# Kernel optimization log

Hardware: AMD Instinct MI355X
Metric: run time of the kernel (lower is better)

Reference implementation:

```python
import jax, jax.numpy as jnp
import numpy as np

NUM_HEADS = 16
HEAD_DIM = 128
NUM_KV_HEADS = 8
NUM_KV_GROUPS = 2
HIDDEN = 2048
SCALE = 0.5  # hardcoded in the original SDPA call


def _fixed_sincos_pos(E, H):
    # matches ReusedProjReconstructor._fixed_sincos_pos (H even here)
    half = H // 2
    freq = jnp.exp(-jnp.log(jnp.float32(10000.0)) * jnp.arange(half, dtype=jnp.float32) / half)
    pos = jnp.arange(E, dtype=jnp.float32)[:, None]
    ang = pos * freq[None, :]
    return jnp.concatenate([jnp.sin(ang), jnp.cos(ang)], axis=1)  # [E, H]


def setup_inputs() -> dict:
    key = jax.random.key(0)
    ks = jax.random.split(key, 8)
    B, M, H = 4, 2048, HIDDEN
    kv_dim = NUM_KV_HEADS * HEAD_DIM
    s = 0.02
    return {
        "mem_act": jax.random.normal(ks[0], (B, M, H), jnp.float32),
        "Wq": jax.random.normal(ks[1], (H, H), jnp.float32) * s,
        "bq": jax.random.normal(ks[2], (H,), jnp.float32) * s,
        "Wk": jax.random.normal(ks[3], (kv_dim, H), jnp.float32) * s,
        "bk": jax.random.normal(ks[4], (kv_dim,), jnp.float32) * s,
        "Wv": jax.random.normal(ks[5], (kv_dim, H), jnp.float32) * s,
        "bv": jax.random.normal(ks[6], (kv_dim,), jnp.float32) * s,
        "Wo": jax.random.normal(ks[7], (H, H), jnp.float32) * s,
        "E": 2048,
    }


def reference(mem_act, Wq, bq, Wk, bk, Wv, bv, Wo, E):
    B, M, H = mem_act.shape
    # positional query hidden, shared across batch (q_ln is Identity)
    q_hidden = _fixed_sincos_pos(E, H).astype(mem_act.dtype)  # [E, H]
    q = (q_hidden @ Wq.T + bq).reshape(E, NUM_HEADS, HEAD_DIM)          # [E, nh, hd]
    k = (mem_act @ Wk.T + bk).reshape(B, M, NUM_KV_HEADS, HEAD_DIM)     # [B, M, nkv, hd]
    v = (mem_act @ Wv.T + bv).reshape(B, M, NUM_KV_HEADS, HEAD_DIM)
    # GQA: repeat kv heads (repeat_interleave over head dim)
    k = jnp.repeat(k, NUM_KV_GROUPS, axis=2)  # [B, M, nh, hd]
    v = jnp.repeat(v, NUM_KV_GROUPS, axis=2)
    # non-causal SDPA with scale=0.5, query broadcast over batch
    scores = jnp.einsum("ehd,bmhd->bhem", q, k) * SCALE  # [B, nh, E, M]
    attn = jax.nn.softmax(scores, axis=-1)
    out = jnp.einsum("bhem,bmhd->behd", attn, v).reshape(B, E, H)
    pred = out @ Wo.T  # o_proj (no bias, Qwen2 style)
    return pred
```

## Files before the change

### kernel.cpp

```cpp
#include <hip/hip_runtime.h>
#include <hip/hip_bf16.h>

typedef __attribute__((ext_vector_type(8))) short short8;
typedef __attribute__((ext_vector_type(4))) float f32x4;
typedef __attribute__((ext_vector_type(16))) float f32x16;
typedef unsigned short ushort_t;

__device__ __forceinline__ unsigned short f2bf(float x) {
    unsigned int u = __builtin_bit_cast(unsigned int, x);
    unsigned int r = (u + 0x7fffu + ((u >> 16) & 1u)) >> 16;
    return (unsigned short)r;
}

__device__ __forceinline__ void gload_lds16(const ushort_t* g, ushort_t* l) {
    __builtin_amdgcn_global_load_lds(
        (const __attribute__((address_space(1))) void*)g,
        (__attribute__((address_space(3))) void*)l, 16, 0, 0);
}

#define MFMA16(A, B, C) __builtin_amdgcn_mfma_f32_16x16x32_bf16((A), (B), (C), 0, 0, 0)
#define MFMA32(A, B, C) __builtin_amdgcn_mfma_f32_32x32x16_bf16((A), (B), (C), 0, 0, 0)

__global__ __launch_bounds__(256) void prep_all(const float* __restrict__ im,
                                                const float* __restrict__ iq,
                                                const float* __restrict__ ik,
                                                const float* __restrict__ iv,
                                                const float* __restrict__ io,
                                                ushort_t* __restrict__ om,
                                                ushort_t* __restrict__ oq,
                                                ushort_t* __restrict__ ok,
                                                ushort_t* __restrict__ ov,
                                                ushort_t* __restrict__ oo,
                                                ushort_t* __restrict__ qh) {
    const int bid = blockIdx.x;
    if (bid < 14336) {
        long i = ((long)bid * 256 + threadIdx.x) << 3;
        const float* s;
        ushort_t* d;
        if (i < 16777216)      { s = im + i;              d = om + i; }
        else if (i < 20971520) { s = iq + (i - 16777216); d = oq + (i - 16777216); }
        else if (i < 23068672) { s = ik + (i - 20971520); d = ok + (i - 20971520); }
        else if (i < 25165824) { s = iv + (i - 23068672); d = ov + (i - 23068672); }
        else                   { s = io + (i - 25165824); d = oo + (i - 25165824); }
        const float4* p = (const float4*)s;
        float4 a = p[0], b = p[1];
        short8 o;
        o[0] = (short)f2bf(a.x); o[1] = (short)f2bf(a.y);
        o[2] = (short)f2bf(a.z); o[3] = (short)f2bf(a.w);
        o[4] = (short)f2bf(b.x); o[5] = (short)f2bf(b.y);
        o[6] = (short)f2bf(b.z); o[7] = (short)f2bf(b.w);
        *(short8*)d = o;
    } else {
        int idx = (bid - 14336) * 256 + threadIdx.x;
        int e = idx >> 10, i = idx & 1023;
        float freq = __expf(-9.2103403719761836f * (float)i * (1.0f / 1024.0f));
        float ang = (float)e * freq;
        float rev = ang * 0.15915494309189535f;
        rev -= floorf(rev);
        float sv, cv;
        asm("v_sin_f32 %0, %1" : "=v"(sv) : "v"(rev));
        asm("v_cos_f32 %0, %1" : "=v"(cv) : "v"(rev));
        qh[(size_t)e * 2048 + i]        = f2bf(sv);
        qh[(size_t)e * 2048 + 1024 + i] = f2bf(cv);
    }
}

__global__ __launch_bounds__(256, 2) void gemm_q(const ushort_t* __restrict__ A,
                                                 const ushort_t* __restrict__ Bw,
                                                 const float* __restrict__ bias,
                                                 ushort_t* __restrict__ Cout,
                                                 int M, int N, int K) {
    __shared__ ushort_t As[4][128 * 32];
    __shared__ ushort_t Bs[4][128 * 32];
    const int tid = threadIdx.x, lane = tid & 63;
    const int wid = tid >> 6;
    const int q5 = lane & 31, hi = lane >> 5;
    const int wm = wid >> 1, wn = wid & 1;
    const int nbn = N >> 7;
    const int nwg = gridDim.x;
    const int swz = (blockIdx.x & 7) * (nwg >> 3) + (blockIdx.x >> 3);
    const int bm = swz / nbn, bn = swz % nbn;
    const int row0 = bm << 7, col0 = bn << 7;
    const int NT = K >> 5;

    f32x16 acc[2][2];
#pragma unroll
    for (int mi = 0; mi < 2; ++mi)
#pragma unroll
        for (int nj = 0; nj < 2; ++nj)
#pragma unroll
            for (int rr = 0; rr < 16; ++rr) acc[mi][nj][rr] = 0.f;

    auto STAGE_HALF = [&](int buf, int kt, int i) {
        const int k0 = kt << 5;
        const int fb = (i * 256 + tid) << 4;
        const int rp = fb >> 7;
        const int bo = ((fb >> 4) & 7) ^ (rp & 7);
        const int row = rp * 2 + (bo >> 2);
        const int kc = (bo & 3) << 3;
        gload_lds16(A  + (size_t)(row0 + row) * K + k0 + kc, &As[buf][0] + (fb >> 1));
        gload_lds16(Bw + (size_t)(col0 + row) * K + k0 + kc, &Bs[buf][0] + (fb >> 1));
    };

    STAGE_HALF(0, 0, 0); STAGE_HALF(0, 0, 1);
    STAGE_HALF(1, 1, 0); STAGE_HALF(1, 1, 1);
    STAGE_HALF(2, 2, 0); STAGE_HALF(2, 2, 1);
    asm volatile("s_waitcnt vmcnt(8)" ::: "memory");
    __builtin_amdgcn_sched_barrier(0);
    __builtin_amdgcn_s_barrier();
    __builtin_amdgcn_sched_barrier(0);

    for (int t = 0; t < NT; ++t) {
        const int buf = t & 3;
        const char* Ab = (const char*)&As[buf][0];
        const char* Bb = (const char*)&Bs[buf][0];
#pragma unroll
        for (int ph = 0; ph < 2; ++ph) {
            short8 af[2], bfr[2];
#pragma unroll
            for (int nj = 0; nj < 2; ++nj) {
                const int col = wn * 64 + nj * 32 + q5;
                const int rp = col >> 1;
                const int blk = (((col & 1) << 2) + ph * 2 + hi) ^ (rp & 7);
                bfr[nj] = *(const short8*)(Bb + rp * 128 + blk * 16);
            }
#pragma unroll
            for (int mi = 0; mi < 2; ++mi) {
                const int row = wm * 64 + mi * 32 + q5;
                const int rp = row >> 1;
                const int blk = (((row & 1) << 2) + ph * 2 + hi) ^ (rp & 7);
                af[mi] = *(const short8*)(Ab + rp * 128 + blk * 16);
            }
            if (t + 3 < NT) STAGE_HALF((t + 3) & 3, t + 3, ph);
            __builtin_amdgcn_s_setprio(1);
#pragma unroll
            for (int mi = 0; mi < 2; ++mi)
#pragma unroll
                for (int nj = 0; nj < 2; ++nj)
                    acc[mi][nj] = MFMA32(af[mi], bfr[nj], acc[mi][nj]);
            __builtin_amdgcn_s_setprio(0);
        }

        if (t + 3 < NT) {
            asm volatile("s_waitcnt vmcnt(8)" ::: "memory");
        } else if (t + 2 < NT) {
            asm volatile("s_waitcnt vmcnt(4)" ::: "memory");
        } else if (t + 1 < NT) {
            asm volatile("s_waitcnt vmcnt(0)" ::: "memory");
        }
        if (t + 1 < NT) {
            __builtin_amdgcn_sched_barrier(0);
            __builtin_amdgcn_s_barrier();
            __builtin_amdgcn_sched_barrier(0);
        }
    }

#pragma unroll
    for (int mi = 0; mi < 2; ++mi)
#pragma unroll
        for (int nj = 0; nj < 2; ++nj) {
            const int col = col0 + wn * 64 + nj * 32 + q5;
            const float bv = bias[col];
#pragma unroll
            for (int rr = 0; rr < 16; ++rr) {
                const int row = row0 + wm * 64 + mi * 32 + (rr & 3) + 8 * (rr >> 2) + 4 * hi;
                Cout[(size_t)row * N + col] = f2bf((acc[mi][nj][rr] + bv) * 0.5f);
            }
        }
}

template <int EPI>
__global__ __launch_bounds__(512, 1) void gemm256(const ushort_t* __restrict__ A,
                                                  const ushort_t* __restrict__ Bw,
                                                  const float* __restrict__ b0,
                                                  const float* __restrict__ b1,
                                                  void* __restrict__ C0,
                                                  void* __restrict__ C1,
                                                  int M, int N, int K) {
    __shared__ ushort_t As[4][256 * 32];
    __shared__ ushort_t Bs[4][256 * 32];
    const int tid = threadIdx.x, lane = tid & 63;
    const int wid = tid >> 6;
    const int q5 = lane & 31, hi = lane >> 5;
    const int wm = wid >> 2, wn = wid & 3;
    const int nbn = N >> 8;
    const int nwg = gridDim.x;
    const int swz = (blockIdx.x & 7) * (nwg >> 3) + (blockIdx.x >> 3);
    const int bm = swz / nbn, bn = swz % nbn;
    const int row0 = bm << 8, col0 = bn << 8;
    const int NT = K >> 5;

    f32x16 acc[4][2];
#pragma unroll
    for (int mi = 0; mi < 4; ++mi)
#pragma unroll
        for (int nj = 0; nj < 2; ++nj)
#pragma unroll
            for (int rr = 0; rr < 16; ++rr) acc[mi][nj][rr] = 0.f;

    auto STAGE_HALF = [&](int buf, int kt, int i) {
        const int k0 = kt << 5;
        const int fb = (i * 512 + tid) << 4;
        const int rp = fb >> 7;
        const int bo = ((fb >> 4) & 7) ^ (rp & 7);
        const int row = rp * 2 + (bo >> 2);
        const int kc = (bo & 3) << 3;
        gload_lds16(A  + (size_t)(row0 + row) * K + k0 + kc, &As[buf][0] + (fb >> 1));
        gload_lds16(Bw + (size_t)(col0 + row) * K + k0 + kc, &Bs[buf][0] + (fb >> 1));
    };

    STAGE_HALF(0, 0, 0); STAGE_HALF(0, 0, 1);
    STAGE_HALF(1, 1, 0); STAGE_HALF(1, 1, 1);
    STAGE_HALF(2, 2, 0); STAGE_HALF(2, 2, 1);
    asm volatile("s_waitcnt vmcnt(8)" ::: "memory");
    __builtin_amdgcn_sched_barrier(0);
    __builtin_amdgcn_s_barrier();
    __builtin_amdgcn_sched_barrier(0);

    for (int t = 0; t < NT; ++t) {
        const int buf = t & 3;
        const char* Ab = (const char*)&As[buf][0];
        const char* Bb = (const char*)&Bs[buf][0];
#pragma unroll
        for (int ph = 0; ph < 2; ++ph) {
            short8 af[4], bfr[2];
#pragma unroll
            for (int nj = 0; nj < 2; ++nj) {
                const int col = wn * 64 + nj * 32 + q5;
                const int rp = col >> 1;
                const int blk = (((col & 1) << 2) + ph * 2 + hi) ^ (rp & 7);
                bfr[nj] = *(const short8*)(Bb + rp * 128 + blk * 16);
            }
#pragma unroll
            for (int mi = 0; mi < 4; ++mi) {
                const int row = wm * 128 + mi * 32 + q5;
                const int rp = row >> 1;
                const int blk = (((row & 1) << 2) + ph * 2 + hi) ^ (rp & 7);
                af[mi] = *(const short8*)(Ab + rp * 128 + blk * 16);
            }
            if (t + 3 < NT) STAGE_HALF((t + 3) & 3, t + 3, ph);
            __builtin_amdgcn_s_setprio(1);
#pragma unroll
            for (int mi = 0; mi < 4; ++mi)
#pragma unroll
                for (int nj = 0; nj < 2; ++nj)
                    acc[mi][nj] = MFMA32(af[mi], bfr[nj], acc[mi][nj]);
            __builtin_amdgcn_s_setprio(0);
        }

        if (t + 3 < NT) {
            asm volatile("s_waitcnt vmcnt(8)" ::: "memory");
        } else if (t + 2 < NT) {
            asm volatile("s_waitcnt vmcnt(4)" ::: "memory");
        } else if (t + 1 < NT) {
            asm volatile("s_waitcnt vmcnt(0)" ::: "memory");
        }
        if (t + 1 < NT) {
            __builtin_amdgcn_sched_barrier(0);
            __builtin_amdgcn_s_barrier();
            __builtin_amdgcn_sched_barrier(0);
        }
    }

#pragma unroll
    for (int mi = 0; mi < 4; ++mi)
#pragma unroll
        for (int nj = 0; nj < 2; ++nj) {
            const int col = col0 + wn * 64 + nj * 32 + q5;
            if (EPI == 2) {
                float* outp = (float*)C0;
#pragma unroll
                for (int rr = 0; rr < 16; ++rr) {
                    const int row = row0 + wm * 128 + mi * 32 + (rr & 3) + 8 * (rr >> 2) + 4 * hi;
                    outp[(size_t)row * N + col] = acc[mi][nj][rr];
                }
            } else {
                if (col < 1024) {
                    const float bv = b0[col];
                    ushort_t* Kp = (ushort_t*)C0;
#pragma unroll
                    for (int rr = 0; rr < 16; ++rr) {
                        const int row = row0 + wm * 128 + mi * 32 + (rr & 3) + 8 * (rr >> 2) + 4 * hi;
                        Kp[(size_t)row * 1024 + col] = f2bf(acc[mi][nj][rr] + bv);
                    }
                } else {
                    const int vcol = col - 1024;
                    const float bv = b1[vcol];
                    ushort_t* Vt = (ushort_t*)C1;
#pragma unroll
                    for (int G = 0; G < 4; ++G) {
                        const int m0 = row0 + wm * 128 + mi * 32 + G * 8 + 4 * hi;
                        const int bb = m0 >> 11;
                        const int mm = m0 & 2047;
                        const size_t vtrow = (size_t)(bb * 8 + (vcol >> 7)) * 128 + (vcol & 127);
                        unsigned int p0 = (unsigned int)f2bf(acc[mi][nj][G * 4 + 0] + bv)
                                        | ((unsigned int)f2bf(acc[mi][nj][G * 4 + 1] + bv) << 16);
                        unsigned int p1 = (unsigned int)f2bf(acc[mi][nj][G * 4 + 2] + bv)
                                        | ((unsigned int)f2bf(acc[mi][nj][G * 4 + 3] + bv) << 16);
                        uint2 pk; pk.x = p0; pk.y = p1;
                        *(uint2*)(Vt + vtrow * 2048 + mm) = pk;
                    }
                }
            }
        }
}

__global__ __launch_bounds__(512, 2) void attn_kernel(const ushort_t* __restrict__ Q,
                                                      const ushort_t* __restrict__ Kg,
                                                      const ushort_t* __restrict__ Vt,
                                                      ushort_t* __restrict__ O) {
    __shared__ ushort_t Ks[2][64 * 128];
    __shared__ ushort_t Vts[2][128 * 64];

    const int tid = threadIdx.x, lane = tid & 63, wid = tid >> 6;
    const int q5 = lane & 31;
    const int hi = lane >> 5;
    const int wq = wid & 3;
    const int wg = (blockIdx.x & 7) * 64 + (blockIdx.x >> 3);
    const int bkvh = wg >> 4;
    const int etile = wg & 15;
    const int b = bkvh >> 3, kvh = bkvh & 7;
    const int h = kvh * 2 + (wid >> 2);
    const int e0 = etile * 128;
    const int qrow = e0 + wq * 32 + q5;

    short8 Qf[8];
    {
        const ushort_t* qp = Q + (size_t)qrow * 2048 + h * 128 + hi * 8;
#pragma unroll
        for (int c = 0; c < 8; ++c) Qf[c] = *(const short8*)(qp + c * 16);
    }

    unsigned aK[2][8];
#pragma unroll
    for (int h2 = 0; h2 < 2; ++h2) {
        const int key = h2 * 32 + q5;
#pragma unroll
        for (int c = 0; c < 8; ++c)
            aK[h2][c] = key * 256 + (((c * 2 + hi) ^ (key & 7)) << 4);
    }
    unsigned aV[4];
#pragma unroll
    for (int c16 = 0; c16 < 4; ++c16)
        aV[c16] = q5 * 128 + (((c16 * 2 + hi) ^ (q5 & 7)) << 4);

    float lrow = 0.f;
    f32x16 oacc[4];
#pragma unroll
    for (int d0 = 0; d0 < 4; ++d0)
#pragma unroll
        for (int r = 0; r < 16; ++r) oacc[d0][r] = 0.f;

    f32x16 Z16;
#pragma unroll
    for (int r = 0; r < 16; ++r) Z16[r] = 0.f;

    const ushort_t* Kbase  = Kg + (size_t)b * 2048 * 1024 + kvh * 128;
    const ushort_t* Vtbase = Vt + (size_t)bkvh * 128 * 2048;

    auto STAGE = [&](int buf, int kv0) {
#pragma unroll
        for (int i = 0; i < 2; ++i) {
            const int fb = (i * 8 + wid) * 1024 + lane * 16;
            const int key = fb >> 8;
            const int blk = (fb >> 4) & 15;
            gload_lds16(Kbase + (size_t)(kv0 + key) * 1024 + ((blk ^ (key & 7)) << 3),
                        &Ks[buf][0] + (fb >> 1));
            const int d = fb >> 7;
            const int kb = (fb >> 4) & 7;
            gload_lds16(Vtbase + (size_t)d * 2048 + kv0 + ((kb ^ (d & 7)) << 3),
                        &Vts[buf][0] + (fb >> 1));
        }
    };

    auto TILE = [&](int bo) {
        f32x16 sS[2];
        __builtin_amdgcn_s_setprio(1);
#pragma unroll
        for (int c = 0; c < 8; ++c) {
            short8 ka0 = *(const short8*)((const char*)Ks + bo + aK[0][c]);
            short8 ka1 = *(const short8*)((const char*)Ks + bo + aK[1][c]);
            sS[0] = MFMA32(ka0, Qf[c], (c == 0) ? Z16 : sS[0]);
            sS[1] = MFMA32(ka1, Qf[c], (c == 0) ? Z16 : sS[1]);
        }
        __builtin_amdgcn_s_setprio(0);

#pragma unroll
        for (int h2 = 0; h2 < 2; ++h2)
#pragma unroll
            for (int r = 0; r < 16; ++r) sS[h2][r] = __expf(sS[h2][r]);

        float ts[16];
#pragma unroll
        for (int i = 0; i < 8; ++i) ts[i] = sS[0][2 * i] + sS[0][2 * i + 1];
#pragma unroll
        for (int i = 0; i < 8; ++i) ts[8 + i] = sS[1][2 * i] + sS[1][2 * i + 1];
#pragma unroll
        for (int s = 8; s > 0; s >>= 1)
#pragma unroll
            for (int i = 0; i < s; ++i) ts[i] += ts[i + s];
        lrow += ts[0] + __shfl_xor(ts[0], 32);

        unsigned int W[2][4][2];
#pragma unroll
        for (int h2 = 0; h2 < 2; ++h2)
#pragma unroll
            for (int q4 = 0; q4 < 4; ++q4)
#pragma unroll
                for (int p = 0; p < 2; ++p) {
                    unsigned int w;
                    asm("v_cvt_pk_bf16_f32 %0, %1, %2"
                        : "=v"(w)
                        : "v"(sS[h2][q4 * 4 + 2 * p]), "v"(sS[h2][q4 * 4 + 2 * p + 1]));
                    W[h2][q4][p] = w;
                }

#pragma unroll
        for (int c16 = 0; c16 < 4; ++c16) {
            const int h2 = c16 >> 1;
            const int q4a = (c16 & 1) * 2, q4b = q4a + 1;
            auto r0 = __builtin_amdgcn_permlane32_swap(W[h2][q4a][0], W[h2][q4b][0], false, false);
            auto r1 = __builtin_amdgcn_permlane32_swap(W[h2][q4a][1], W[h2][q4b][1], false, false);
            union { unsigned int w[4]; short8 v; } pa;
            pa.w[0] = r0[0];
            pa.w[1] = r1[0];
            pa.w[2] = r0[1];
            pa.w[3] = r1[1];
            __builtin_amdgcn_s_setprio(1);
#pragma unroll
            for (int d0 = 0; d0 < 4; ++d0) {
                short8 vb = *(const short8*)((const char*)Vts + bo + aV[c16] + d0 * 4096);
                oacc[d0] = MFMA32(pa.v, vb, oacc[d0]);
            }
            __builtin_amdgcn_s_setprio(0);
        }
    };

    STAGE(0, 0);
    __syncthreads();

#pragma unroll 1
    for (int tt = 0; tt < 16; ++tt) {
        STAGE(1, (2 * tt + 1) * 64);
        TILE(0);
        __syncthreads();
        if (tt < 15) STAGE(0, (2 * tt + 2) * 64);
        TILE(16384);
        __syncthreads();
    }

#pragma unroll
    for (int reg = 0; reg < 16; ++reg) {
        const int qr = (reg & 3) + 8 * (reg >> 2) + 4 * hi;
        const float lr = __shfl(lrow, qr);
        const float inv = 1.0f / lr;
        const int e = e0 + wq * 32 + qr;
        ushort_t* op = O + ((size_t)b * 2048 + e) * 2048 + h * 128 + q5;
#pragma unroll
        for (int d0 = 0; d0 < 4; ++d0)
            op[d0 * 32] = f2bf(oacc[d0][reg] * inv);
    }
}

extern "C" void kernel_launch(void* const* d_in, const int* in_sizes, int n_in,
                              void* d_out, int out_size, void* d_ws, size_t ws_size,
                              hipStream_t stream) {
    const float* mem_act = (const float*)d_in[0];
    const float* Wq = (const float*)d_in[1];
    const float* bq = (const float*)d_in[2];
    const float* Wk = (const float*)d_in[3];
    const float* bk = (const float*)d_in[4];
    const float* Wv = (const float*)d_in[5];
    const float* bv = (const float*)d_in[6];
    const float* Wo = (const float*)d_in[7];
    float* out = (float*)d_out;

    char* w = (char*)d_ws;
    ushort_t* memb = (ushort_t*)w; w += (size_t)16777216 * 2;
    ushort_t* wqb  = (ushort_t*)w; w += (size_t)4194304 * 2;
    ushort_t* wkvb = (ushort_t*)w; w += (size_t)4194304 * 2;
    ushort_t* wob  = (ushort_t*)w; w += (size_t)4194304 * 2;
    ushort_t* qh   = (ushort_t*)w; w += (size_t)4194304 * 2;
    ushort_t* Qp   = (ushort_t*)w; w += (size_t)4194304 * 2;
    ushort_t* Kp   = (ushort_t*)w; w += (size_t)8388608 * 2;
    ushort_t* Vtp  = (ushort_t*)w; w += (size_t)8388608 * 2;
    ushort_t* AO   = (ushort_t*)w; w += (size_t)16777216 * 2;

    dim3 blk(256);
    prep_all<<<22528, blk, 0, stream>>>(mem_act, Wq, Wk, Wv, Wo,
                                        memb, wqb, wkvb, wkvb + (size_t)2097152, wob, qh);

    gemm_q<<<16 * 16, blk, 0, stream>>>(qh, wqb, bq, Qp, 2048, 2048, 2048);

    gemm256<0><<<256, dim3(512), 0, stream>>>(memb, wkvb, bk, bv, Kp, Vtp, 8192, 2048, 2048);

    attn_kernel<<<512, dim3(512), 0, stream>>>(Qp, Kp, Vtp, AO);

    gemm256<2><<<256, dim3(512), 0, stream>>>(AO, wob, nullptr, nullptr, out, nullptr, 8192, 2048, 2048);
}
```

Measured before the change: 363.3 us.

## Restructure attention so each wave handles two query groups sharing K/V fragments

The attention kernel moves from 512-thread blocks covering two heads of a KV pair to 256-thread blocks covering one head. Each wave now owns 64 query rows as two 32-row groups, so every K and V LDS fragment read feeds two MFMAs. This is meant to halve LDS read traffic per MFMA and raise arithmetic intensity per wave. The cost is doubled accumulator and Q registers, which may cut occupancy, and K/V tiles are no longer shared across the two GQA heads within a block, so global/L2 K/V traffic increases.

```diff
diff --git a/kernel.cpp b/kernel.cpp
--- a/kernel.cpp
+++ b/kernel.cpp
@@ -305,7 +305,7 @@
         }
 }
 
-__global__ __launch_bounds__(512, 2) void attn_kernel(const ushort_t* __restrict__ Q,
+__global__ __launch_bounds__(256, 2) void attn_kernel(const ushort_t* __restrict__ Q,
                                                       const ushort_t* __restrict__ Kg,
                                                       const ushort_t* __restrict__ Vt,
                                                       ushort_t* __restrict__ O) {
@@ -315,53 +315,45 @@
     const int tid = threadIdx.x, lane = tid & 63, wid = tid >> 6;
     const int q5 = lane & 31;
     const int hi = lane >> 5;
-    const int wq = wid & 3;
     const int wg = (blockIdx.x & 7) * 64 + (blockIdx.x >> 3);
-    const int bkvh = wg >> 4;
-    const int etile = wg & 15;
-    const int b = bkvh >> 3, kvh = bkvh & 7;
-    const int h = kvh * 2 + (wid >> 2);
-    const int e0 = etile * 128;
-    const int qrow = e0 + wq * 32 + q5;
-
-    short8 Qf[8];
-    {
-        const ushort_t* qp = Q + (size_t)qrow * 2048 + h * 128 + hi * 8;
-#pragma unroll
-        for (int c = 0; c < 8; ++c) Qf[c] = *(const short8*)(qp + c * 16);
+    const int bh = wg >> 3;
+    const int chunk = wg & 7;
+    const int b = bh >> 4, h = bh & 15, kvh = h >> 1;
+    const int e0 = chunk * 256 + wid * 64;
+
+    short8 Qf[2][8];
+#pragma unroll
+    for (int qg = 0; qg < 2; ++qg) {
+        const ushort_t* qp = Q + (size_t)(e0 + qg * 32 + q5) * 2048 + h * 128 + hi * 8;
+#pragma unroll
+        for (int c = 0; c < 8; ++c) Qf[qg][c] = *(const short8*)(qp + c * 16);
     }
 
-    unsigned aK[2][8];
-#pragma unroll
-    for (int h2 = 0; h2 < 2; ++h2) {
-        const int key = h2 * 32 + q5;
-#pragma unroll
-        for (int c = 0; c < 8; ++c)
-            aK[h2][c] = key * 256 + (((c * 2 + hi) ^ (key & 7)) << 4);
-    }
+    unsigned aK[8];
+#pragma unroll
+    for (int c = 0; c < 8; ++c)
+        aK[c] = q5 * 256 + (((c * 2 + hi) ^ (q5 & 7)) << 4);
     unsigned aV[4];
 #pragma unroll
     for (int c16 = 0; c16 < 4; ++c16)
         aV[c16] = q5 * 128 + (((c16 * 2 + hi) ^ (q5 & 7)) << 4);
 
-    float lrow = 0.f;
-    f32x16 oacc[4];
-#pragma unroll
-    for (int d0 = 0; d0 < 4; ++d0)
-#pragma unroll
-        for (int r = 0; r < 16; ++r) oacc[d0][r] = 0.f;
-
-    f32x16 Z16;
-#pragma unroll
-    for (int r = 0; r < 16; ++r) Z16[r] = 0.f;
+    float lrow[2] = {0.f, 0.f};
+    f32x16 oacc[2][4];
+#pragma unroll
+    for (int qg = 0; qg < 2; ++qg)
+#pragma unroll
+        for (int d0 = 0; d0 < 4; ++d0)
+#pragma unroll
+            for (int r = 0; r < 16; ++r) oacc[qg][d0][r] = 0.f;
 
     const ushort_t* Kbase  = Kg + (size_t)b * 2048 * 1024 + kvh * 128;
-    const ushort_t* Vtbase = Vt + (size_t)bkvh * 128 * 2048;
+    const ushort_t* Vtbase = Vt + (size_t)(b * 8 + kvh) * 128 * 2048;
 
     auto STAGE = [&](int buf, int kv0) {
 #pragma unroll
-        for (int i = 0; i < 2; ++i) {
-            const int fb = (i * 8 + wid) * 1024 + lane * 16;
+        for (int i = 0; i < 4; ++i) {
+            const int fb = (i * 4 + wid) * 1024 + lane * 16;
             const int key = fb >> 8;
             const int blk = (fb >> 4) & 15;
             gload_lds16(Kbase + (size_t)(kv0 + key) * 1024 + ((blk ^ (key & 7)) << 3),
@@ -374,65 +366,69 @@
     };
 
     auto TILE = [&](int bo) {
-        f32x16 sS[2];
-        __builtin_amdgcn_s_setprio(1);
-#pragma unroll
-        for (int c = 0; c < 8; ++c) {
-            short8 ka0 = *(const short8*)((const char*)Ks + bo + aK[0][c]);
-            short8 ka1 = *(const short8*)((const char*)Ks + bo + aK[1][c]);
-            sS[0] = MFMA32(ka0, Qf[c], (c == 0) ? Z16 : sS[0]);
-            sS[1] = MFMA32(ka1, Qf[c], (c == 0) ? Z16 : sS[1]);
-        }
-        __builtin_amdgcn_s_setprio(0);
-
-#pragma unroll
-        for (int h2 = 0; h2 < 2; ++h2)
-#pragma unroll
-            for (int r = 0; r < 16; ++r) sS[h2][r] = __expf(sS[h2][r]);
-
-        float ts[16];
-#pragma unroll
-        for (int i = 0; i < 8; ++i) ts[i] = sS[0][2 * i] + sS[0][2 * i + 1];
-#pragma unroll
-        for (int i = 0; i < 8; ++i) ts[8 + i] = sS[1][2 * i] + sS[1][2 * i + 1];
-#pragma unroll
-        for (int s = 8; s > 0; s >>= 1)
-#pragma unroll
-            for (int i = 0; i < s; ++i) ts[i] += ts[i + s];
-        lrow += ts[0] + __shfl_xor(ts[0], 32);
-
-        unsigned int W[2][4][2];
-#pragma unroll
-        for (int h2 = 0; h2 < 2; ++h2)
-#pragma unroll
-            for (int q4 = 0; q4 < 4; ++q4)
-#pragma unroll
-                for (int p = 0; p < 2; ++p) {
-                    unsigned int w;
-                    asm("v_cvt_pk_bf16_f32 %0, %1, %2"
-                        : "=v"(w)
-                        : "v"(sS[h2][q4 * 4 + 2 * p]), "v"(sS[h2][q4 * 4 + 2 * p + 1]));
-                    W[h2][q4][p] = w;
+#pragma unroll
+        for (int h2 = 0; h2 < 2; ++h2) {
+            f32x16 s0, s1;
+#pragma unroll
+            for (int r = 0; r < 16; ++r) { s0[r] = 0.f; s1[r] = 0.f; }
+            __builtin_amdgcn_s_setprio(1);
+#pragma unroll
+            for (int c = 0; c < 8; ++c) {
+                short8 ka = *(const short8*)((const char*)Ks + bo + h2 * 8192 + aK[c]);
+                s0 = MFMA32(ka, Qf[0][c], s0);
+                s1 = MFMA32(ka, Qf[1][c], s1);
+            }
+            __builtin_amdgcn_s_setprio(0);
+
+#pragma unroll
+            for (int r = 0; r < 16; ++r) { s0[r] = __expf(s0[r]); s1[r] = __expf(s1[r]); }
+            {
+                float ta[8], tb[8];
+#pragma unroll
+                for (int i = 0; i < 8; ++i) { ta[i] = s0[2 * i] + s0[2 * i + 1];
+                                              tb[i] = s1[2 * i] + s1[2 * i + 1]; }
+#pragma unroll
+                for (int s = 4; s > 0; s >>= 1)
+#pragma unroll
+                    for (int i = 0; i < s; ++i) { ta[i] += ta[i + s]; tb[i] += tb[i + s]; }
+                lrow[0] += ta[0] + __shfl_xor(ta[0], 32);
+                lrow[1] += tb[0] + __shfl_xor(tb[0], 32);
+            }
+
+#pragma unroll
+            for (int cc = 0; cc < 2; ++cc) {
+                const int c16 = h2 * 2 + cc;
+                const int q4a = cc * 2, q4b = cc * 2 + 1;
+                union { unsigned int w[4]; short8 v; } pa0, pa1;
+                {
+                    unsigned int w0a, w0b, w1a, w1b;
+                    asm("v_cvt_pk_bf16_f32 %0, %1, %2" : "=v"(w0a) : "v"(s0[q4a * 4 + 0]), "v"(s0[q4a * 4 + 1]));
+                    asm("v_cvt_pk_bf16_f32 %0, %1, %2" : "=v"(w0b) : "v"(s0[q4a * 4 + 2]), "v"(s0[q4a * 4 + 3]));
+                    asm("v_cvt_pk_bf16_f32 %0, %1, %2" : "=v"(w1a) : "v"(s0[q4b * 4 + 0]), "v"(s0[q4b * 4 + 1]));
+                    asm("v_cvt_pk_bf16_f32 %0, %1, %2" : "=v"(w1b) : "v"(s0[q4b * 4 + 2]), "v"(s0[q4b * 4 + 3]));
+                    auto r0 = __builtin_amdgcn_permlane32_swap(w0a, w1a, false, false);
+                    auto r1 = __builtin_amdgcn_permlane32_swap(w0b, w1b, false, false);
+                    pa0.w[0] = r0[0]; pa0.w[1] = r1[0]; pa0.w[2] = r0[1]; pa0.w[3] = r1[1];
                 }
-
-#pragma unroll
-        for (int c16 = 0; c16 < 4; ++c16) {
-            const int h2 = c16 >> 1;
-            const int q4a = (c16 & 1) * 2, q4b = q4a + 1;
-            auto r0 = __builtin_amdgcn_permlane32_swap(W[h2][q4a][0], W[h2][q4b][0], false, false);
-            auto r1 = __builtin_amdgcn_permlane32_swap(W[h2][q4a][1], W[h2][q4b][1], false, false);
-            union { unsigned int w[4]; short8 v; } pa;
-            pa.w[0] = r0[0];
-            pa.w[1] = r1[0];
-            pa.w[2] = r0[1];
-            pa.w[3] = r1[1];
-            __builtin_amdgcn_s_setprio(1);
-#pragma unroll
-            for (int d0 = 0; d0 < 4; ++d0) {
-                short8 vb = *(const short8*)((const char*)Vts + bo + aV[c16] + d0 * 4096);
-                oacc[d0] = MFMA32(pa.v, vb, oacc[d0]);
-            }
-            __builtin_amdgcn_s_setprio(0);
+                {
+                    unsigned int w0a, w0b, w1a, w1b;
+                    asm("v_cvt_pk_bf16_f32 %0, %1, %2" : "=v"(w0a) : "v"(s1[q4a * 4 + 0]), "v"(s1[q4a * 4 + 1]));
+                    asm("v_cvt_pk_bf16_f32 %0, %1, %2" : "=v"(w0b) : "v"(s1[q4a * 4 + 2]), "v"(s1[q4a * 4 + 3]));
+                    asm("v_cvt_pk_bf16_f32 %0, %1, %2" : "=v"(w1a) : "v"(s1[q4b * 4 + 0]), "v"(s1[q4b * 4 + 1]));
+                    asm("v_cvt_pk_bf16_f32 %0, %1, %2" : "=v"(w1b) : "v"(s1[q4b * 4 + 2]), "v"(s1[q4b * 4 + 3]));
+                    auto r0 = __builtin_amdgcn_permlane32_swap(w0a, w1a, false, false);
+                    auto r1 = __builtin_amdgcn_permlane32_swap(w0b, w1b, false, false);
+                    pa1.w[0] = r0[0]; pa1.w[1] = r1[0]; pa1.w[2] = r0[1]; pa1.w[3] = r1[1];
+                }
+                __builtin_amdgcn_s_setprio(1);
+#pragma unroll
+                for (int d0 = 0; d0 < 4; ++d0) {
+                    short8 vb = *(const short8*)((const char*)Vts + bo + aV[c16] + d0 * 4096);
+                    oacc[0][d0] = MFMA32(pa0.v, vb, oacc[0][d0]);
+                    oacc[1][d0] = MFMA32(pa1.v, vb, oacc[1][d0]);
+                }
+                __builtin_amdgcn_s_setprio(0);
+            }
         }
     };
 
@@ -450,16 +446,18 @@
     }
 
 #pragma unroll
-    for (int reg = 0; reg < 16; ++reg) {
-        const int qr = (reg & 3) + 8 * (reg >> 2) + 4 * hi;
-        const float lr = __shfl(lrow, qr);
-        const float inv = 1.0f / lr;
-        const int e = e0 + wq * 32 + qr;
-        ushort_t* op = O + ((size_t)b * 2048 + e) * 2048 + h * 128 + q5;
-#pragma unroll
-        for (int d0 = 0; d0 < 4; ++d0)
-            op[d0 * 32] = f2bf(oacc[d0][reg] * inv);
-    }
+    for (int qg = 0; qg < 2; ++qg)
+#pragma unroll
+        for (int reg = 0; reg < 16; ++reg) {
+            const int qr = (reg & 3) + 8 * (reg >> 2) + 4 * hi;
+            const float lr = __shfl(lrow[qg], qr);
+            const float inv = 1.0f / lr;
+            const int e = e0 + qg * 32 + qr;
+            ushort_t* op = O + ((size_t)b * 2048 + e) * 2048 + h * 128 + q5;
+#pragma unroll
+            for (int d0 = 0; d0 < 4; ++d0)
+                op[d0 * 32] = f2bf(oacc[qg][d0][reg] * inv);
+        }
 }
 
 extern "C" void kernel_launch(void* const* d_in, const int* in_sizes, int n_in,
@@ -494,7 +492,7 @@
 
     gemm256<0><<<256, dim3(512), 0, stream>>>(memb, wkvb, bk, bv, Kp, Vtp, 8192, 2048, 2048);
 
-    attn_kernel<<<512, dim3(512), 0, stream>>>(Qp, Kp, Vtp, AO);
+    attn_kernel<<<512, blk, 0, stream>>>(Qp, Kp, Vtp, AO);
 
     gemm256<2><<<256, dim3(512), 0, stream>>>(AO, wob, nullptr, nullptr, out, nullptr, 8192, 2048, 2048);
 }
```

Result: slower. 587.7 us (+61.8%).
